# Performance work log

Hardware: AMD Instinct MI355X
Metric: run time of the kernel (lower is better)

The kernel has to match this reference:

```python
import jax, jax.numpy as jnp
import numpy as np

N_NODES = 100000
N_EDGES = 800000
DIMS = [(768, 64), (64, 32), (32, 16), (16, 5)]


def setup_inputs() -> dict:
    key = jax.random.key(0)
    ks = jax.random.split(key, 3 + 3 * len(DIMS))
    inp = {
        "x": jax.random.normal(ks[0], (N_NODES, DIMS[0][0]), jnp.float32),
        "edge_index": jax.random.randint(ks[1], (2, N_EDGES), 0, N_NODES),
        "edge_weight": jax.random.uniform(ks[2], (N_EDGES,), jnp.float32),
    }
    for i, (di, do) in enumerate(DIMS, start=1):
        s = 1.0 / np.sqrt(di)
        k0, k1, k2 = ks[3 * i], ks[3 * i + 1], ks[3 * i + 2]
        inp[f"W{i}l"] = jax.random.uniform(k0, (di, do), jnp.float32, -s, s)
        inp[f"W{i}r"] = jax.random.uniform(k1, (di, do), jnp.float32, -s, s)
        inp[f"b{i}"] = jax.random.uniform(k2, (do,), jnp.float32, -s, s)
    return inp


def _sage_conv(h, src, dst, inv_deg, Wl, Wr, b):
    # SAGEConv (mean aggregation): lin_l(mean_{j->i} h_j) + lin_r(h_i)
    agg = jax.ops.segment_sum(h[src], dst, num_segments=h.shape[0]) * inv_deg[:, None]
    return agg @ Wl + h @ Wr + b


def reference(x, edge_index, edge_weight,
              W1l, W1r, b1, W2l, W2r, b2, W3l, W3r, b3, W4l, W4r, b4):
    # edge_weight is accepted (matches original forward) but PyG SAGEConv mean
    # aggregation ignores it. Dropout is identity (deterministic eval reference).
    src, dst = edge_index[0], edge_index[1]
    deg = jax.ops.segment_sum(jnp.ones((src.shape[0],), x.dtype), dst,
                              num_segments=x.shape[0])
    inv_deg = jnp.where(deg > 0, 1.0 / deg, 0.0)
    h = jax.nn.relu(_sage_conv(x, src, dst, inv_deg, W1l, W1r, b1))
    h = jax.nn.relu(_sage_conv(h, src, dst, inv_deg, W2l, W2r, b2))
    h = jax.nn.relu(_sage_conv(h, src, dst, inv_deg, W3l, W3r, b3))
    return _sage_conv(h, src, dst, inv_deg, W4l, W4r, b4)
```

## Files before the change

### kernel.cpp

```cpp
#include <hip/hip_runtime.h>

using half8 = __attribute__((ext_vector_type(8))) _Float16;
using f32x4 = __attribute__((ext_vector_type(4))) float;

typedef __attribute__((address_space(3))) unsigned int lds_uint;
typedef __attribute__((address_space(1))) const unsigned int glb_uint;
__device__ __forceinline__ void async_copy16(const void* g, void* l) {
  __builtin_amdgcn_global_load_lds((glb_uint*)g, (lds_uint*)l, 16, 0, 0);
}

__device__ __forceinline__ void raw_barrier() {
  asm volatile("" ::: "memory");
  __builtin_amdgcn_s_barrier();
  asm volatile("" ::: "memory");
}

__global__ void prep_zero_kernel(const float* __restrict__ W1l, const float* __restrict__ W1r,
                                 const float* __restrict__ W2l, const float* __restrict__ W2r,
                                 const float* __restrict__ W3l, const float* __restrict__ W3r,
                                 const float* __restrict__ W4l, const float* __restrict__ W4r,
                                 _Float16* __restrict__ w1, _Float16* __restrict__ w2,
                                 _Float16* __restrict__ w3, _Float16* __restrict__ w4,
                                 int4* __restrict__ zp, int n4) {
  int i = blockIdx.x * 256 + threadIdx.x;
  if (i < 98304) {
    int c = i / 768, k = i - c * 768;
    float v = (c < 64) ? W1l[k * 64 + c] : W1r[k * 64 + (c - 64)];
    w1[i] = (_Float16)v;
  } else if (i < 98304 + 4096) {
    int j = i - 98304;
    int c = j >> 6, k = j & 63;
    float v = (c < 32) ? W2l[k * 32 + c] : W2r[k * 32 + (c - 32)];
    w2[j] = (_Float16)v;
  } else if (i < 98304 + 4096 + 1024) {
    int j = i - (98304 + 4096);
    int c = j >> 5, k = j & 31;
    float v = (c < 16) ? W3l[k * 16 + c] : W3r[k * 16 + (c - 16)];
    w3[j] = (_Float16)v;
  } else if (i < 98304 + 4096 + 1024 + 512) {
    int j = i - (98304 + 4096 + 1024);
    int c = j >> 5, k = j & 31;
    float v = 0.f;
    if (k < 16) {
      if (c < 5) v = W4l[k * 5 + c];
      else if (c < 10) v = W4r[k * 5 + (c - 5)];
    }
    w4[j] = (_Float16)v;
  } else {
    int j = i - (98304 + 4096 + 1024 + 512);
    if (j < n4) zp[j] = make_int4(0, 0, 0, 0);
  }
}

__global__ void deg_kernel(const int* __restrict__ dst, int* __restrict__ cnt, int e) {
  int i = blockIdx.x * 256 + threadIdx.x;
  if (i < e) atomicAdd(&cnt[dst[i]], 1);
}

__global__ void scan1_kernel(const int* __restrict__ cnt, int* __restrict__ off,
                             int* __restrict__ bsum, float* __restrict__ invd, int nodes) {
  __shared__ int sh[256];
  int tid = threadIdx.x;
  int base = blockIdx.x * 1024 + tid * 4;
  int a0 = (base + 0 < nodes) ? cnt[base + 0] : 0;
  int a1 = (base + 1 < nodes) ? cnt[base + 1] : 0;
  int a2 = (base + 2 < nodes) ? cnt[base + 2] : 0;
  int a3 = (base + 3 < nodes) ? cnt[base + 3] : 0;
  if (base + 0 < nodes) invd[base + 0] = a0 > 0 ? 1.0f / (float)a0 : 0.f;
  if (base + 1 < nodes) invd[base + 1] = a1 > 0 ? 1.0f / (float)a1 : 0.f;
  if (base + 2 < nodes) invd[base + 2] = a2 > 0 ? 1.0f / (float)a2 : 0.f;
  if (base + 3 < nodes) invd[base + 3] = a3 > 0 ? 1.0f / (float)a3 : 0.f;
  int s3 = a0 + a1 + a2 + a3;
  sh[tid] = s3;
  __syncthreads();
  for (int d = 1; d < 256; d <<= 1) {
    int v = (tid >= d) ? sh[tid - d] : 0;
    __syncthreads();
    sh[tid] += v;
    __syncthreads();
  }
  int excl = sh[tid] - s3;
  if (base + 0 <= nodes) off[base + 0] = excl;
  if (base + 1 <= nodes) off[base + 1] = excl + a0;
  if (base + 2 <= nodes) off[base + 2] = excl + a0 + a1;
  if (base + 3 <= nodes) off[base + 3] = excl + a0 + a1 + a2;
  if (tid == 255) bsum[blockIdx.x] = sh[255];
}

__global__ void scan2_kernel(int* __restrict__ bsum, int nb) {
  __shared__ int sh[128];
  int tid = threadIdx.x;
  int v = (tid < nb) ? bsum[tid] : 0;
  sh[tid] = v;
  __syncthreads();
  for (int d = 1; d < 128; d <<= 1) {
    int u = (tid >= d) ? sh[tid - d] : 0;
    __syncthreads();
    sh[tid] += u;
    __syncthreads();
  }
  if (tid < nb) bsum[tid] = sh[tid] - v;
}

__global__ void scan3_kernel(int* __restrict__ off, const int* __restrict__ bsum, int ntot) {
  int i = blockIdx.x * 256 + threadIdx.x;
  if (i < ntot) off[i] += bsum[i >> 10];
}

__global__ void sortfill_kernel(const int* __restrict__ src, const int* __restrict__ dst,
                                const int* __restrict__ off, int* __restrict__ cur,
                                int* __restrict__ csr, int e) {
  int i = blockIdx.x * 256 + threadIdx.x;
  if (i < e) {
    int d = dst[i];
    int pos = atomicAdd(&cur[d], 1);
    csr[off[d] + pos] = src[i];
  }
}

__global__ __launch_bounds__(256, 3) void gemm1_kernel(
    const float* __restrict__ x,
    const _Float16* __restrict__ w16,
    const float* __restrict__ bias,
    _Float16* __restrict__ p, _Float16* __restrict__ q, int n) {
  constexpr int DI = 768, BK = 32, NT = DI / BK;
  __shared__ float aS[2][128 * BK];
  __shared__ _Float16 bS[2][128 * BK];
  int t = threadIdx.x;
  int lane = t & 63, w = t >> 6;
  int lm = lane & 15, lk = lane >> 4;
  int m0 = blockIdx.x * 128;

  const float* agp[4];
  int abase[4];
#pragma unroll
  for (int j = 0; j < 4; ++j) {
    int g = (j * 4 + w) * 64 + lane;
    int row = g >> 3, gi = g & 7;
    int gj = gi ^ (row & 7);
    int grow = m0 + row;
    if (grow >= n) grow = n - 1;
    agp[j] = x + (size_t)grow * DI + gj * 4;
    abase[j] = (j * 4 + w) * 256;
  }
  const _Float16* bgp[2];
  int bbase[2];
#pragma unroll
  for (int j = 0; j < 2; ++j) {
    int g = (j * 4 + w) * 64 + lane;
    int c = g >> 2, gi = g & 3;
    int gj = gi ^ ((c >> 1) & 3);
    bgp[j] = w16 + (size_t)c * DI + gj * 8;
    bbase[j] = (j * 4 + w) * 512;
  }

  f32x4 acc[2][8];
#pragma unroll
  for (int mi = 0; mi < 2; ++mi)
#pragma unroll
    for (int ni = 0; ni < 8; ++ni) acc[mi][ni] = (f32x4){0.f, 0.f, 0.f, 0.f};

  int r0l = w * 32 + lm, r1l = r0l + 16;
  int sw = lm & 7;
  int bsw = (lk ^ ((lm >> 1) & 3)) << 3;

  auto compute_tile = [&](const float* ab, const _Float16* bb) {
    f32x4 v0a = *(const f32x4*)(ab + r0l * 32 + (((lk * 2 + 0) ^ sw) << 2));
    f32x4 v0b = *(const f32x4*)(ab + r0l * 32 + (((lk * 2 + 1) ^ sw) << 2));
    f32x4 v1a = *(const f32x4*)(ab + r1l * 32 + (((lk * 2 + 0) ^ sw) << 2));
    f32x4 v1b = *(const f32x4*)(ab + r1l * 32 + (((lk * 2 + 1) ^ sw) << 2));
    half8 a0, a1;
#pragma unroll
    for (int j = 0; j < 4; ++j) {
      a0[j] = (_Float16)v0a[j]; a0[4 + j] = (_Float16)v0b[j];
      a1[j] = (_Float16)v1a[j]; a1[4 + j] = (_Float16)v1b[j];
    }
#pragma unroll
    for (int ni = 0; ni < 8; ++ni) {
      half8 b = *(const half8*)(bb + ni * 512 + lm * 32 + bsw);
      acc[0][ni] = __builtin_amdgcn_mfma_f32_16x16x32_f16(a0, b, acc[0][ni], 0, 0, 0);
      acc[1][ni] = __builtin_amdgcn_mfma_f32_16x16x32_f16(a1, b, acc[1][ni], 0, 0, 0);
    }
  };

#pragma unroll
  for (int j = 0; j < 4; ++j) async_copy16(agp[j], &aS[0][abase[j]]);
#pragma unroll
  for (int j = 0; j < 2; ++j) async_copy16(bgp[j], &bS[0][bbase[j]]);

  for (int ts = 0; ts < NT - 1; ++ts) {
    int cur = ts & 1;
    int kc = (ts + 1) * BK;
#pragma unroll
    for (int j = 0; j < 4; ++j) async_copy16(agp[j] + kc, &aS[cur ^ 1][abase[j]]);
#pragma unroll
    for (int j = 0; j < 2; ++j) async_copy16(bgp[j] + kc, &bS[cur ^ 1][bbase[j]]);
    asm volatile("s_waitcnt vmcnt(6)" ::: "memory");
    raw_barrier();
    compute_tile(aS[cur], bS[cur]);
    raw_barrier();
  }
  asm volatile("s_waitcnt vmcnt(0)" ::: "memory");
  raw_barrier();
  compute_tile(aS[(NT - 1) & 1], bS[(NT - 1) & 1]);

#pragma unroll
  for (int mi = 0; mi < 2; ++mi)
#pragma unroll
    for (int ni = 0; ni < 8; ++ni) {
      int col = ni * 16 + lm;
#pragma unroll
      for (int j = 0; j < 4; ++j) {
        int row = m0 + w * 32 + mi * 16 + lk * 4 + j;
        if (row < n) {
          float v = acc[mi][ni][j];
          if (col < 64) p[(size_t)row * 64 + col] = (_Float16)v;
          else q[(size_t)row * 64 + (col - 64)] = (_Float16)(v + bias[col - 64]);
        }
      }
    }
}

template <int DIR, int DIP, int PSI, int NC, int NCR, int DO, int PSO>
__global__ __launch_bounds__(512) void fused_agg_gemm_kernel(
    const _Float16* __restrict__ pin, const _Float16* __restrict__ qin,
    const int* __restrict__ off, const int* __restrict__ csr, const float* __restrict__ invd,
    const _Float16* __restrict__ w16, const float* __restrict__ bias,
    _Float16* __restrict__ pout, _Float16* __restrict__ qout, int n) {
  constexpr int SP = DIP + 8;
  constexpr int C8 = DIR / 8;
  constexpr int ACT = (C8 >= 4) ? 4 : C8;
  constexpr int CQ = C8 / ACT;
  constexpr int NF = NC / 16;
  __shared__ _Float16 hs[128 * SP];
  int t = threadIdx.x;
  int node_l = t >> 2, q4 = t & 3;
  int node = blockIdx.x * 128 + node_l;

  if (node < n) {
    if (q4 < ACT) {
      int e0 = off[node], e1 = off[node + 1];
      const half8* p8 = (const half8*)pin;
      float s[CQ][8];
#pragma unroll
      for (int c = 0; c < CQ; ++c)
#pragma unroll
        for (int j = 0; j < 8; ++j) s[c][j] = 0.f;
      int e = e0;
      for (; e + 2 <= e1; e += 2) {
        int i0 = csr[e], i1 = csr[e + 1];
        half8 v0[CQ], v1[CQ];
#pragma unroll
        for (int c = 0; c < CQ; ++c) v0[c] = p8[(size_t)i0 * PSI + q4 * CQ + c];
#pragma unroll
        for (int c = 0; c < CQ; ++c) v1[c] = p8[(size_t)i1 * PSI + q4 * CQ + c];
#pragma unroll
        for (int c = 0; c < CQ; ++c)
#pragma unroll
          for (int j = 0; j < 8; ++j) {
            s[c][j] += (float)v0[c][j];
            s[c][j] += (float)v1[c][j];
          }
      }
      if (e < e1) {
        int i0 = csr[e];
#pragma unroll
        for (int c = 0; c < CQ; ++c) {
          half8 v = p8[(size_t)i0 * PSI + q4 * CQ + c];
#pragma unroll
          for (int j = 0; j < 8; ++j) s[c][j] += (float)v[j];
        }
      }
      float id = invd[node];
#pragma unroll
      for (int c = 0; c < CQ; ++c) {
        half8 qv = ((const half8*)qin)[(size_t)node * PSI + q4 * CQ + c];
        half8 o;
#pragma unroll
        for (int j = 0; j < 8; ++j) o[j] = (_Float16)fmaxf(s[c][j] * id + (float)qv[j], 0.f);
        *(half8*)(hs + node_l * SP + (q4 * CQ + c) * 8) = o;
      }
    } else if (DIP > DIR && (q4 - ACT) < (DIP - DIR) / 8) {
      half8 z = {};
      *(half8*)(hs + node_l * SP + (C8 + (q4 - ACT)) * 8) = z;
    }
  }
  __syncthreads();

  int lane = t & 63, w = t >> 6;
  int lm = lane & 15, lk = lane >> 4;
  int row_l = w * 16 + lm;
  const _Float16* wp = w16 + (size_t)lm * DIP + lk * 8;
  f32x4 acc[NF];
#pragma unroll
  for (int ni = 0; ni < NF; ++ni) acc[ni] = (f32x4){0.f, 0.f, 0.f, 0.f};
#pragma unroll
  for (int kc = 0; kc < DIP; kc += 32) {
    half8 a = *(const half8*)(hs + row_l * SP + kc + lk * 8);
#pragma unroll
    for (int ni = 0; ni < NF; ++ni) {
      half8 b = *(const half8*)(wp + (size_t)ni * 16 * DIP + kc);
      acc[ni] = __builtin_amdgcn_mfma_f32_16x16x32_f16(a, b, acc[ni], 0, 0, 0);
    }
  }
#pragma unroll
  for (int ni = 0; ni < NF; ++ni) {
    int col = ni * 16 + lm;
    if (col >= NCR) continue;
#pragma unroll
    for (int j = 0; j < 4; ++j) {
      int row = blockIdx.x * 128 + w * 16 + lk * 4 + j;
      if (row < n) {
        float v = acc[ni][j];
        if (col < DO) pout[(size_t)row * PSO + col] = (_Float16)v;
        else qout[(size_t)row * PSO + (col - DO)] = (_Float16)(v + bias[col - DO]);
      }
    }
  }
}

__global__ __launch_bounds__(256) void aggregate_last_kernel(
    const _Float16* __restrict__ p, const _Float16* __restrict__ q,
    const int* __restrict__ off, const int* __restrict__ csr,
    const float* __restrict__ invd, float* __restrict__ out, int n) {
  int node = blockIdx.x * 256 + threadIdx.x;
  if (node >= n) return;
  int e0 = off[node], e1 = off[node + 1];
  const half8* p8 = (const half8*)p;
  float s[8];
#pragma unroll
  for (int j = 0; j < 8; ++j) s[j] = 0.f;
  int e = e0;
  for (; e + 2 <= e1; e += 2) {
    half8 v0 = p8[csr[e]];
    half8 v1 = p8[csr[e + 1]];
#pragma unroll
    for (int j = 0; j < 8; ++j) {
      s[j] += (float)v0[j];
      s[j] += (float)v1[j];
    }
  }
  if (e < e1) {
    half8 v = p8[csr[e]];
#pragma unroll
    for (int j = 0; j < 8; ++j) s[j] += (float)v[j];
  }
  float id = invd[node];
  half8 qv = ((const half8*)q)[node];
#pragma unroll
  for (int j = 0; j < 5; ++j) out[(size_t)node * 5 + j] = s[j] * id + (float)qv[j];
}

extern "C" void kernel_launch(void* const* d_in, const int* in_sizes, int n_in,
                              void* d_out, int out_size, void* d_ws, size_t ws_size,
                              hipStream_t stream) {
  const float* x = (const float*)d_in[0];
  const int* ei = (const int*)d_in[1];
  const int E = in_sizes[1] / 2;
  const int* esrc = ei;
  const int* edst = ei + E;
  const float* W1l = (const float*)d_in[3];
  const float* W1r = (const float*)d_in[4];
  const float* b1 = (const float*)d_in[5];
  const float* W2l = (const float*)d_in[6];
  const float* W2r = (const float*)d_in[7];
  const float* b2 = (const float*)d_in[8];
  const float* W3l = (const float*)d_in[9];
  const float* W3r = (const float*)d_in[10];
  const float* b3 = (const float*)d_in[11];
  const float* W4l = (const float*)d_in[12];
  const float* W4r = (const float*)d_in[13];
  const float* b4 = (const float*)d_in[14];
  const int N = in_sizes[0] / 768;
  float* out = (float*)d_out;
  (void)n_in; (void)out_size; (void)ws_size;

  char* base = (char*)d_ws;
  size_t o = 0;
  auto alloc = [&](size_t bytes) -> void* {
    void* ptr = base + o;
    o = (o + bytes + 255) & ~(size_t)255;
    return ptr;
  };
  int* cnt = (int*)alloc((size_t)2 * N * 4);
  int* cur = cnt + N;
  int* off = (int*)alloc((size_t)(N + 1) * 4);
  int* bsum = (int*)alloc(1024);
  int* csr = (int*)alloc((size_t)E * 4);
  float* invd = (float*)alloc((size_t)N * 4);
  _Float16* w1 = (_Float16*)alloc((size_t)128 * 768 * 2);
  _Float16* w2 = (_Float16*)alloc((size_t)64 * 64 * 2);
  _Float16* w3 = (_Float16*)alloc((size_t)32 * 32 * 2);
  _Float16* w4 = (_Float16*)alloc((size_t)16 * 32 * 2);
  _Float16* P1 = (_Float16*)alloc((size_t)N * 64 * 2);
  _Float16* Q1 = (_Float16*)alloc((size_t)N * 64 * 2);
  _Float16* P2 = (_Float16*)alloc((size_t)N * 32 * 2);
  _Float16* Q2 = (_Float16*)alloc((size_t)N * 32 * 2);
  _Float16* P3 = (_Float16*)alloc((size_t)N * 16 * 2);
  _Float16* Q3 = (_Float16*)alloc((size_t)N * 16 * 2);
  _Float16* P4 = (_Float16*)alloc((size_t)N * 8 * 2);
  _Float16* Q4 = (_Float16*)alloc((size_t)N * 8 * 2);

  const int n4 = (2 * N + 3) / 4;
  const int prep_tot = 98304 + 4096 + 1024 + 512 + n4;
  prep_zero_kernel<<<(prep_tot + 255) / 256, 256, 0, stream>>>(
      W1l, W1r, W2l, W2r, W3l, W3r, W4l, W4r, w1, w2, w3, w4, (int4*)cnt, n4);

  deg_kernel<<<(E + 255) / 256, 256, 0, stream>>>(edst, cnt, E);
  const int nb = (N + 1 + 1023) / 1024;
  scan1_kernel<<<nb, 256, 0, stream>>>(cnt, off, bsum, invd, N);
  scan2_kernel<<<1, 128, 0, stream>>>(bsum, nb);
  scan3_kernel<<<(N + 1 + 255) / 256, 256, 0, stream>>>(off, bsum, N + 1);
  sortfill_kernel<<<(E + 255) / 256, 256, 0, stream>>>(esrc, edst, off, cur, csr, E);

  gemm1_kernel<<<(N + 127) / 128, 256, 0, stream>>>(x, w1, b1, P1, Q1, N);
  const int gb = (N + 127) / 128;
  fused_agg_gemm_kernel<64, 64, 8, 64, 64, 32, 32>
      <<<gb, 512, 0, stream>>>(P1, Q1, off, csr, invd, w2, b2, P2, Q2, N);
  fused_agg_gemm_kernel<32, 32, 4, 32, 32, 16, 16>
      <<<gb, 512, 0, stream>>>(P2, Q2, off, csr, invd, w3, b3, P3, Q3, N);
  fused_agg_gemm_kernel<16, 32, 2, 16, 10, 5, 8>
      <<<gb, 512, 0, stream>>>(P3, Q3, off, csr, invd, w4, b4, P4, Q4, N);
  aggregate_last_kernel<<<(N + 255) / 256, 256, 0, stream>>>(P4, Q4, off, csr, invd, out, N);
}
```

Baseline: 255.7 us.

## Merge CSR fill into GEMM1 launch and parallelize aggregation across edges per wave

The CSR sort-fill is folded into the first GEMM kernel as extra blocks, so both run in one launch and the fill can overlap the GEMM. The aggregation in the fused agg+GEMM kernels now gives each node a whole wave: lanes split the node's edges and feature chunks, and a shuffle-xor reduction combines the partial sums. The last aggregation likewise uses 8 lanes per node. This raises memory-level parallelism for the irregular gathers, but lanes sit idle on low-degree nodes and the extra shuffles add work.

```diff
diff --git a/kernel.cpp b/kernel.cpp
--- a/kernel.cpp
+++ b/kernel.cpp
@@ -107,22 +107,20 @@
   if (i < ntot) off[i] += bsum[i >> 10];
 }
 
-__global__ void sortfill_kernel(const int* __restrict__ src, const int* __restrict__ dst,
-                                const int* __restrict__ off, int* __restrict__ cur,
-                                int* __restrict__ csr, int e) {
-  int i = blockIdx.x * 256 + threadIdx.x;
-  if (i < e) {
-    int d = dst[i];
-    int pos = atomicAdd(&cur[d], 1);
-    csr[off[d] + pos] = src[i];
-  }
-}
-
-__global__ __launch_bounds__(256, 3) void gemm1_kernel(
-    const float* __restrict__ x,
-    const _Float16* __restrict__ w16,
-    const float* __restrict__ bias,
-    _Float16* __restrict__ p, _Float16* __restrict__ q, int n) {
+__global__ __launch_bounds__(256, 3) void gemm1_sortfill_kernel(
+    const float* __restrict__ x, const _Float16* __restrict__ w16,
+    const float* __restrict__ bias, _Float16* __restrict__ p, _Float16* __restrict__ q,
+    int n, int gemm_gb, const int* __restrict__ esrc, const int* __restrict__ edst,
+    const int* __restrict__ off, int* __restrict__ cur, int* __restrict__ csr, int E) {
+  if ((int)blockIdx.x >= gemm_gb) {
+    int i = ((int)blockIdx.x - gemm_gb) * 256 + threadIdx.x;
+    if (i < E) {
+      int d = edst[i];
+      int pos = atomicAdd(&cur[d], 1);
+      csr[off[d] + pos] = esrc[i];
+    }
+    return;
+  }
   constexpr int DI = 768, BK = 32, NT = DI / BK;
   __shared__ float aS[2][128 * BK];
   __shared__ _Float16 bS[2][128 * BK];
@@ -189,15 +187,15 @@
   for (int j = 0; j < 2; ++j) async_copy16(bgp[j], &bS[0][bbase[j]]);
 
   for (int ts = 0; ts < NT - 1; ++ts) {
-    int cur = ts & 1;
+    int cur2 = ts & 1;
     int kc = (ts + 1) * BK;
 #pragma unroll
-    for (int j = 0; j < 4; ++j) async_copy16(agp[j] + kc, &aS[cur ^ 1][abase[j]]);
-#pragma unroll
-    for (int j = 0; j < 2; ++j) async_copy16(bgp[j] + kc, &bS[cur ^ 1][bbase[j]]);
+    for (int j = 0; j < 4; ++j) async_copy16(agp[j] + kc, &aS[cur2 ^ 1][abase[j]]);
+#pragma unroll
+    for (int j = 0; j < 2; ++j) async_copy16(bgp[j] + kc, &bS[cur2 ^ 1][bbase[j]]);
     asm volatile("s_waitcnt vmcnt(6)" ::: "memory");
     raw_barrier();
-    compute_tile(aS[cur], bS[cur]);
+    compute_tile(aS[cur2], bS[cur2]);
     raw_barrier();
   }
   asm volatile("s_waitcnt vmcnt(0)" ::: "memory");
@@ -229,65 +227,52 @@
     _Float16* __restrict__ pout, _Float16* __restrict__ qout, int n) {
   constexpr int SP = DIP + 8;
   constexpr int C8 = DIR / 8;
-  constexpr int ACT = (C8 >= 4) ? 4 : C8;
-  constexpr int CQ = C8 / ACT;
+  constexpr int LOG2C8 = (C8 == 8) ? 3 : ((C8 == 4) ? 2 : 1);
+  constexpr int EPAR = 64 / C8;
   constexpr int NF = NC / 16;
   __shared__ _Float16 hs[128 * SP];
   int t = threadIdx.x;
-  int node_l = t >> 2, q4 = t & 3;
-  int node = blockIdx.x * 128 + node_l;
-
-  if (node < n) {
-    if (q4 < ACT) {
+  int lane = t & 63, w = t >> 6;
+  int chunk = lane & (C8 - 1);
+  int e_sub = lane >> LOG2C8;
+  const half8* p8 = (const half8*)pin;
+
+  for (int i = w; i < 128; i += 8) {
+    int node = blockIdx.x * 128 + i;
+    if (node < n) {
       int e0 = off[node], e1 = off[node + 1];
-      const half8* p8 = (const half8*)pin;
-      float s[CQ][8];
-#pragma unroll
-      for (int c = 0; c < CQ; ++c)
-#pragma unroll
-        for (int j = 0; j < 8; ++j) s[c][j] = 0.f;
-      int e = e0;
-      for (; e + 2 <= e1; e += 2) {
-        int i0 = csr[e], i1 = csr[e + 1];
-        half8 v0[CQ], v1[CQ];
-#pragma unroll
-        for (int c = 0; c < CQ; ++c) v0[c] = p8[(size_t)i0 * PSI + q4 * CQ + c];
-#pragma unroll
-        for (int c = 0; c < CQ; ++c) v1[c] = p8[(size_t)i1 * PSI + q4 * CQ + c];
-#pragma unroll
-        for (int c = 0; c < CQ; ++c)
-#pragma unroll
-          for (int j = 0; j < 8; ++j) {
-            s[c][j] += (float)v0[c][j];
-            s[c][j] += (float)v1[c][j];
-          }
-      }
-      if (e < e1) {
-        int i0 = csr[e];
-#pragma unroll
-        for (int c = 0; c < CQ; ++c) {
-          half8 v = p8[(size_t)i0 * PSI + q4 * CQ + c];
-#pragma unroll
-          for (int j = 0; j < 8; ++j) s[c][j] += (float)v[j];
+      float s[8];
+#pragma unroll
+      for (int j = 0; j < 8; ++j) s[j] = 0.f;
+      for (int eb = e0; eb < e1; eb += EPAR) {
+        int e = eb + e_sub;
+        if (e < e1) {
+          int src = csr[e];
+          half8 v = p8[(size_t)src * PSI + chunk];
+#pragma unroll
+          for (int j = 0; j < 8; ++j) s[j] += (float)v[j];
         }
       }
-      float id = invd[node];
-#pragma unroll
-      for (int c = 0; c < CQ; ++c) {
-        half8 qv = ((const half8*)qin)[(size_t)node * PSI + q4 * CQ + c];
+#pragma unroll
+      for (int m = C8; m < 64; m <<= 1)
+#pragma unroll
+        for (int j = 0; j < 8; ++j) s[j] += __shfl_xor(s[j], m);
+      if (e_sub == 0) {
+        float id = invd[node];
+        half8 qv = ((const half8*)qin)[(size_t)node * PSI + chunk];
         half8 o;
 #pragma unroll
-        for (int j = 0; j < 8; ++j) o[j] = (_Float16)fmaxf(s[c][j] * id + (float)qv[j], 0.f);
-        *(half8*)(hs + node_l * SP + (q4 * CQ + c) * 8) = o;
+        for (int j = 0; j < 8; ++j) o[j] = (_Float16)fmaxf(s[j] * id + (float)qv[j], 0.f);
+        *(half8*)(hs + i * SP + chunk * 8) = o;
+        if (DIP > DIR) {
+          half8 z = {};
+          *(half8*)(hs + i * SP + (chunk + C8) * 8) = z;
+        }
       }
-    } else if (DIP > DIR && (q4 - ACT) < (DIP - DIR) / 8) {
-      half8 z = {};
-      *(half8*)(hs + node_l * SP + (C8 + (q4 - ACT)) * 8) = z;
     }
   }
   __syncthreads();
 
-  int lane = t & 63, w = t >> 6;
   int lm = lane & 15, lk = lane >> 4;
   int row_l = w * 16 + lm;
   const _Float16* wp = w16 + (size_t)lm * DIP + lk * 8;
@@ -323,32 +308,34 @@
     const _Float16* __restrict__ p, const _Float16* __restrict__ q,
     const int* __restrict__ off, const int* __restrict__ csr,
     const float* __restrict__ invd, float* __restrict__ out, int n) {
-  int node = blockIdx.x * 256 + threadIdx.x;
+  int t = threadIdx.x;
+  int lane = t & 63, w = t >> 6;
+  int node_sub = lane >> 3, e_sub = lane & 7;
+  int node = blockIdx.x * 32 + w * 8 + node_sub;
   if (node >= n) return;
   int e0 = off[node], e1 = off[node + 1];
   const half8* p8 = (const half8*)p;
   float s[8];
 #pragma unroll
   for (int j = 0; j < 8; ++j) s[j] = 0.f;
-  int e = e0;
-  for (; e + 2 <= e1; e += 2) {
-    half8 v0 = p8[csr[e]];
-    half8 v1 = p8[csr[e + 1]];
-#pragma unroll
-    for (int j = 0; j < 8; ++j) {
-      s[j] += (float)v0[j];
-      s[j] += (float)v1[j];
-    }
-  }
-  if (e < e1) {
-    half8 v = p8[csr[e]];
-#pragma unroll
-    for (int j = 0; j < 8; ++j) s[j] += (float)v[j];
-  }
-  float id = invd[node];
-  half8 qv = ((const half8*)q)[node];
-#pragma unroll
-  for (int j = 0; j < 5; ++j) out[(size_t)node * 5 + j] = s[j] * id + (float)qv[j];
+  for (int eb = e0; eb < e1; eb += 8) {
+    int e = eb + e_sub;
+    if (e < e1) {
+      half8 v = p8[csr[e]];
+#pragma unroll
+      for (int j = 0; j < 8; ++j) s[j] += (float)v[j];
+    }
+  }
+#pragma unroll
+  for (int m = 1; m <= 4; m <<= 1)
+#pragma unroll
+    for (int j = 0; j < 8; ++j) s[j] += __shfl_xor(s[j], m);
+  if (e_sub == 0) {
+    float id = invd[node];
+    half8 qv = ((const half8*)q)[node];
+#pragma unroll
+    for (int j = 0; j < 5; ++j) out[(size_t)node * 5 + j] = s[j] * id + (float)qv[j];
+  }
 }
 
 extern "C" void kernel_launch(void* const* d_in, const int* in_sizes, int n_in,
@@ -411,9 +398,12 @@
   scan1_kernel<<<nb, 256, 0, stream>>>(cnt, off, bsum, invd, N);
   scan2_kernel<<<1, 128, 0, stream>>>(bsum, nb);
   scan3_kernel<<<(N + 1 + 255) / 256, 256, 0, stream>>>(off, bsum, N + 1);
-  sortfill_kernel<<<(E + 255) / 256, 256, 0, stream>>>(esrc, edst, off, cur, csr, E);
-
-  gemm1_kernel<<<(N + 127) / 128, 256, 0, stream>>>(x, w1, b1, P1, Q1, N);
+
+  const int gemm_gb = (N + 127) / 128;
+  const int sf_gb = (E + 255) / 256;
+  gemm1_sortfill_kernel<<<gemm_gb + sf_gb, 256, 0, stream>>>(
+      x, w1, b1, P1, Q1, N, gemm_gb, esrc, edst, off, cur, csr, E);
+
   const int gb = (N + 127) / 128;
   fused_agg_gemm_kernel<64, 64, 8, 64, 64, 32, 32>
       <<<gb, 512, 0, stream>>>(P1, Q1, off, csr, invd, w2, b2, P2, Q2, N);
@@ -421,5 +411,5 @@
       <<<gb, 512, 0, stream>>>(P2, Q2, off, csr, invd, w3, b3, P3, Q3, N);
   fused_agg_gemm_kernel<16, 32, 2, 16, 10, 5, 8>
       <<<gb, 512, 0, stream>>>(P3, Q3, off, csr, invd, w4, b4, P4, Q4, N);
-  aggregate_last_kernel<<<(N + 255) / 256, 256, 0, stream>>>(P4, Q4, off, csr, invd, out, N);
-}
+  aggregate_last_kernel<<<(N + 31) / 32, 256, 0, stream>>>(P4, Q4, off, csr, invd, out, N);
+}
```

Result: slower. 359.8 us (+40.7%).
